# Performance work log

Measured on AMD Instinct MI355X. Metric: run time of the kernel, lower is better.

The kernel has to match this reference:

```python
import jax, jax.numpy as jnp
import numpy as np
from jax import lax

B, P, DMAX, DMEL, H = 32, 192, 48, 80, 64
BN_EPS = 1e-5


def setup_inputs() -> dict:
    key = jax.random.key(0)
    ks = jax.random.split(key, 20)
    T = P * DMAX
    s = 0.1
    k_gru = 1.0 / np.sqrt(H)
    inp = {
        "mels": jax.random.normal(ks[0], (B, T, DMEL), jnp.float32),
        # phone durations in frames, in [1, DMAX]
        "durations": jax.random.randint(ks[1], (B, P), 0, DMAX, dtype=jnp.int32) + 1,
        "max_dur": DMAX,
        "conv_w": 1.0 + s * jax.random.normal(ks[2], (2,), jnp.float32),
        "conv_b": s * jax.random.normal(ks[3], (2,), jnp.float32),
        "bn_gamma": 0.5 + jax.random.uniform(ks[4], (2,), jnp.float32),
        "bn_beta": s * jax.random.normal(ks[5], (2,), jnp.float32),
        "bn_mean": s * jax.random.normal(ks[6], (2,), jnp.float32),
        "bn_var": 0.5 + jax.random.uniform(ks[7], (2,), jnp.float32),
        "W_ih_f": k_gru * jax.random.normal(ks[8], (3 * H, DMEL), jnp.float32),
        "W_hh_f": k_gru * jax.random.normal(ks[9], (3 * H, H), jnp.float32),
        "b_ih_f": k_gru * jax.random.normal(ks[10], (3 * H,), jnp.float32),
        "b_hh_f": k_gru * jax.random.normal(ks[11], (3 * H,), jnp.float32),
        "W_ih_b": k_gru * jax.random.normal(ks[12], (3 * H, DMEL), jnp.float32),
        "W_hh_b": k_gru * jax.random.normal(ks[13], (3 * H, H), jnp.float32),
        "b_ih_b": k_gru * jax.random.normal(ks[14], (3 * H,), jnp.float32),
        "b_hh_b": k_gru * jax.random.normal(ks[15], (3 * H,), jnp.float32),
    }
    return inp


def gru_cell(x, h, Wih, Whh, bih, bhh):
    # PyTorch GRU cell convention (gate order r, z, n)
    gi = x @ Wih.T + bih
    gh = h @ Whh.T + bhh
    ir, iz, inn = jnp.split(gi, 3, axis=-1)
    hr, hz, hn = jnp.split(gh, 3, axis=-1)
    r = jax.nn.sigmoid(ir + hr)
    z = jax.nn.sigmoid(iz + hz)
    n = jnp.tanh(inn + r * hn)
    return (1.0 - z) * n + z * h


def reference(mels, durations, max_dur, conv_w, conv_b, bn_gamma, bn_beta,
              bn_mean, bn_var, W_ih_f, W_hh_f, b_ih_f, b_hh_f,
              W_ih_b, W_hh_b, b_ih_b, b_hh_b):
    Bq, T, D = mels.shape
    Pq = durations.shape[1]
    Hq = W_hh_f.shape[1]

    # --- mel2phone: gather each phone's mel segment into [B, P, DMAX, D] ---
    ends = jnp.cumsum(durations, axis=1)
    starts = ends - durations
    t = jnp.arange(max_dur)
    idx = jnp.clip(starts[:, :, None] + t[None, None, :], 0, T - 1)  # [B,P,Dmax]
    segs = mels[jnp.arange(Bq)[:, None, None], idx]                  # [B,P,Dmax,D]
    mask = t[None, None, :] < durations[:, :, None]                  # [B,P,Dmax]

    # --- ConvBNorms2d: 1x1 single-channel conv + eval-mode BN + ReLU, x n_layers ---
    x = segs
    for i in range(conv_w.shape[0]):
        x = conv_w[i] * x + conv_b[i]
        x = (x - bn_mean[i]) * (bn_gamma[i] / jnp.sqrt(bn_var[i] + BN_EPS)) + bn_beta[i]
        x = jax.nn.relu(x)

    # --- per-segment bidirectional GRU, keep last valid timestep ---
    BP = Bq * Pq
    xs = x.reshape(BP, max_dur, D).transpose(1, 0, 2)        # [Dmax, BP, D]
    ms = mask.reshape(BP, max_dur).T                         # [Dmax, BP]

    def step(h, inp):
        xt, mt = inp
        hn = gru_cell(xt, h, W_ih_f, W_hh_f, b_ih_f, b_hh_f)
        h = jnp.where(mt[:, None], hn, h)  # freeze hidden past segment end
        return h, None

    h0 = jnp.zeros((BP, Hq), x.dtype)
    h_fwd, _ = lax.scan(step, h0, (xs, ms))                  # fwd hidden at len-1

    # backward direction output at the last valid position = one GRU step on x[len-1]
    last_idx = jnp.clip(durations - 1, 0, max_dur - 1)       # [B,P]
    x_last = jnp.take_along_axis(x, last_idx[:, :, None, None], axis=2)[:, :, 0, :]
    h_bwd = gru_cell(x_last.reshape(BP, D), h0, W_ih_b, W_hh_b, b_ih_b, b_hh_b)

    out = jnp.concatenate([h_fwd, h_bwd], axis=-1).reshape(Bq, Pq, 2 * Hq)
    out = out * (durations > 0)[:, :, None]  # phone2utter zero-padding
    return out


if __name__ == "__main__":
    o = reference(**setup_inputs())
    print(o.shape, o.dtype)
```

## Files before the change

kernel.cpp:

```cpp
#include <hip/hip_runtime.h>

#define NB 32
#define NP 192
#define DM 48
#define ND 80
#define NH 64
#define NT (NP*DM)
#define NBP (NB*NP)
#define NSG (NBP/16)

typedef _Float16 half8 __attribute__((ext_vector_type(8)));
typedef float f32x4 __attribute__((ext_vector_type(4)));

#define WS_STARTS 0
#define WS_WIH   32768
#define WS_WHH   (32768 + 36864)
#define WS_WIHB  (32768 + 36864 + 24576)

__device__ __forceinline__ float sigm(float x){ return 1.0f/(1.0f + __expf(-x)); }
__device__ __forceinline__ float tanh_f(float x){ return 1.0f - 2.0f/(1.0f + __expf(2.0f*x)); }

__device__ __forceinline__ unsigned packh2(float a, float b){
    unsigned short ua = __builtin_bit_cast(unsigned short, (_Float16)a);
    unsigned short ub = __builtin_bit_cast(unsigned short, (_Float16)b);
    return (unsigned)ua | ((unsigned)ub << 16);
}

struct Aff { float a0,c0,a1,c1; };
__device__ __forceinline__ Aff make_aff(const float* cw, const float* cb, const float* bg,
                                        const float* bb, const float* bm, const float* bv){
    float s0 = bg[0]*rsqrtf(bv[0]+1e-5f);
    float s1 = bg[1]*rsqrtf(bv[1]+1e-5f);
    Aff A;
    A.a0 = cw[0]*s0; A.c0 = (cb[0]-bm[0])*s0 + bb[0];
    A.a1 = cw[1]*s1; A.c1 = (cb[1]-bm[1])*s1 + bb[1];
    return A;
}
__device__ __forceinline__ float aff(float x, const Aff A){
    float y = fmaxf(fmaf(A.a0, x, A.c0), 0.0f);
    return fmaxf(fmaf(A.a1, y, A.c1), 0.0f);
}

__device__ __forceinline__ void lds_barrier(){
    asm volatile("s_waitcnt lgkmcnt(0)" ::: "memory");
    __builtin_amdgcn_s_barrier();
    asm volatile("" ::: "memory");
}

__global__ __launch_bounds__(NP) void k_starts(const int* __restrict__ dur,
                                               int* __restrict__ starts){
    __shared__ int s[NP];
    int b = blockIdx.x, p = threadIdx.x;
    int d = dur[b*NP + p];
    s[p] = d;
    __syncthreads();
    #pragma unroll
    for (int off = 1; off < NP; off <<= 1){
        int v = (p >= off) ? s[p - off] : 0;
        __syncthreads();
        s[p] += v;
        __syncthreads();
    }
    starts[b*NP + p] = s[p] - d;
}

__global__ __launch_bounds__(256) void k_prep(const float* __restrict__ Wih,
                                              const float* __restrict__ Whh,
                                              const float* __restrict__ Wihb,
                                              unsigned short* __restrict__ wih16,
                                              unsigned short* __restrict__ whh16,
                                              unsigned short* __restrict__ wihb16){
    int idx = blockIdx.x*256 + threadIdx.x;
    if (idx < 12*3*64*8){
        int i = idx & 7, l = (idx>>3) & 63, ks = (idx>>9) % 3, f = idx / 1536;
        int j = (f>>2)*64 + (f&3)*16 + (l&15);
        int k = ks*32 + (l>>4)*8 + i;
        float v = (k < ND) ? Wih[j*ND + k] : 0.0f;
        wih16[idx] = __builtin_bit_cast(unsigned short, (_Float16)v);
        return;
    }
    int idx2 = idx - 12*3*64*8;
    if (idx2 < 12*2*64*8){
        int i = idx2 & 7, l = (idx2>>3) & 63, ks = (idx2>>9) & 1, f = idx2 / 1024;
        int j = (f>>2)*64 + (f&3)*16 + (l&15);
        int k = ks*32 + (l>>4)*8 + i;
        whh16[idx2] = __builtin_bit_cast(unsigned short, (_Float16)Whh[j*NH + k]);
        return;
    }
    int idx3 = idx2 - 12*2*64*8;
    if (idx3 < 12*3*64*8){
        int i = idx3 & 7, l = (idx3>>3) & 63, ks = (idx3>>9) % 3, f = idx3 / 1536;
        int j = (f>>2)*64 + (f&3)*16 + (l&15);
        int k = ks*32 + (l>>4)*8 + i;
        float v = (k < ND) ? Wihb[j*ND + k] : 0.0f;
        wihb16[idx3] = __builtin_bit_cast(unsigned short, (_Float16)v);
    }
}

__global__ __launch_bounds__(256, 2) void k_fused(
        const float* __restrict__ mels,
        const int* __restrict__ starts,
        const int* __restrict__ dur,
        const unsigned short* __restrict__ wih16,
        const unsigned short* __restrict__ whh16,
        const unsigned short* __restrict__ wihb16,
        const float* __restrict__ bih,  const float* __restrict__ bhh,
        const float* __restrict__ bihb, const float* __restrict__ bhhb,
        const float* __restrict__ cw, const float* __restrict__ cb,
        const float* __restrict__ bg, const float* __restrict__ bb,
        const float* __restrict__ bm, const float* __restrict__ bv,
        float* __restrict__ out){
    __shared__ alignas(16) uint4 xf[3*192];
    __shared__ alignas(16) uint4 xlast[192];
    __shared__ alignas(16) unsigned short hh2[2*1152];
    __shared__ alignas(16) unsigned short hl2[2*1152];

    int sg  = blockIdx.x;
    int tid = threadIdx.x;
    int w = tid >> 6, l = tid & 63;
    int sc = l & 15, g4 = l >> 4;
    Aff A = make_aff(cw,cb,bg,bb,bm,bv);

    half8 Af[3][3], Ah[3][2];
    #pragma unroll
    for (int gt = 0; gt < 3; ++gt){
        #pragma unroll
        for (int ks = 0; ks < 3; ++ks)
            Af[gt][ks] = *(const half8*)(wih16 + (size_t)(((gt*4+w)*3 + ks)*64 + l)*8);
        #pragma unroll
        for (int ks = 0; ks < 2; ++ks)
            Ah[gt][ks] = *(const half8*)(whh16 + (size_t)(((gt*4+w)*2 + ks)*64 + l)*8);
    }
    f32x4 bi[3], bh[3];
    #pragma unroll
    for (int gt = 0; gt < 3; ++gt){
        float4 t4 = *(const float4*)(bih + gt*64 + w*16 + g4*4);
        bi[gt][0]=t4.x; bi[gt][1]=t4.y; bi[gt][2]=t4.z; bi[gt][3]=t4.w;
        float4 u4 = *(const float4*)(bhh + gt*64 + w*16 + g4*4);
        bh[gt][0]=u4.x; bh[gt][1]=u4.y; bh[gt][2]=u4.z; bh[gt][3]=u4.w;
    }
    int dl_g = dur[sg*16 + sc];

    bool stg = (tid < 192);
    int ks_s = tid >> 6, ls = tid & 63;
    int scs = ls & 15, g4s = ls >> 4;
    int k0 = ks_s*32 + g4s*8;
    bool valid = stg && (k0 < ND);
    int st_s = 0, d_s = -1;
    if (stg){ st_s = starts[sg*16 + scs]; d_s = dur[sg*16 + scs]; }
    const float* mb = mels + (size_t)(sg/12)*NT*ND;

    auto ld2 = [&](int t, float4& va, float4& vb){
        int r = st_s + t; r = (r < NT-1) ? r : (NT-1);
        const float* p = mb + (size_t)r*ND + k0;
        va = *(const float4*)p;
        vb = *(const float4*)(p + 4);
    };
    auto stage = [&](int pw, int tt, float4 va, float4 vb){
        if (valid){
            float y0=aff(va.x,A), y1=aff(va.y,A), y2=aff(va.z,A), y3=aff(va.w,A);
            float y4=aff(vb.x,A), y5=aff(vb.y,A), y6=aff(vb.z,A), y7=aff(vb.w,A);
            uint4 P = uint4{packh2(y0,y1), packh2(y2,y3), packh2(y4,y5), packh2(y6,y7)};
            xf[pw*192 + tid] = P;
            if (tt == d_s - 1) xlast[tid] = P;
        }
    };

    if (stg && !valid){
        uint4 z = uint4{0,0,0,0};
        xf[0*192 + tid] = z; xf[1*192 + tid] = z; xf[2*192 + tid] = z;
        xlast[tid] = z;
    }
    for (int i = tid; i < 288; i += 256){
        ((uint4*)hh2)[i] = uint4{0,0,0,0};
        ((uint4*)hl2)[i] = uint4{0,0,0,0};
    }
    float4 va0 = {0,0,0,0}, vb0 = {0,0,0,0}, va1 = {0,0,0,0}, vb1 = {0,0,0,0};
    if (valid) ld2(0, va0, vb0);
    stage(0, 0, va0, vb0);
    if (valid) ld2(1, va0, vb0);
    float h[4] = {0.f,0.f,0.f,0.f};
    lds_barrier();

#define MFMA(a,b,c) __builtin_amdgcn_mfma_f32_16x16x32_f16(a,b,c,0,0,0)
#define GSTEP(K, SA, SB, LA, LB)                                                      \
{                                                                                     \
    const int PR = (K) % 3, PW = ((K)+1) % 3, HB = (K) & 1;                           \
    const int t = tb + (K);                                                           \
    half8 X0  = *(const half8*)&xf[PR*192 +   0 + l];                                 \
    half8 X1  = *(const half8*)&xf[PR*192 +  64 + l];                                 \
    half8 X2  = *(const half8*)&xf[PR*192 + 128 + l];                                 \
    half8 Hh0 = *(const half8*)&hh2[HB*1152 + sc*72 +  0 + g4*8];                     \
    half8 Hh1 = *(const half8*)&hh2[HB*1152 + sc*72 + 32 + g4*8];                     \
    half8 Hl0 = *(const half8*)&hl2[HB*1152 + sc*72 +  0 + g4*8];                     \
    half8 Hl1 = *(const half8*)&hl2[HB*1152 + sc*72 + 32 + g4*8];                     \
    if (t+1 < DM) stage(PW, t+1, SA, SB);                                             \
    if (valid && (t+2 < DM)) ld2(t+2, LA, LB);                                        \
    f32x4 ga0 = bi[0], ga1 = bi[1], ga2 = bi[2];                                      \
    f32x4 ha0 = bh[0], ha1 = bh[1], ha2 = bh[2];                                      \
    ha0 = MFMA(Ah[0][0], Hh0, ha0); ha1 = MFMA(Ah[1][0], Hh0, ha1);                   \
    ha2 = MFMA(Ah[2][0], Hh0, ha2);                                                   \
    ga0 = MFMA(Af[0][0], X0, ga0);  ga1 = MFMA(Af[1][0], X0, ga1);                    \
    ga2 = MFMA(Af[2][0], X0, ga2);                                                    \
    ha0 = MFMA(Ah[0][0], Hl0, ha0); ha1 = MFMA(Ah[1][0], Hl0, ha1);                   \
    ha2 = MFMA(Ah[2][0], Hl0, ha2);                                                   \
    ga0 = MFMA(Af[0][1], X1, ga0);  ga1 = MFMA(Af[1][1], X1, ga1);                    \
    ga2 = MFMA(Af[2][1], X1, ga2);                                                    \
    ha0 = MFMA(Ah[0][1], Hh1, ha0); ha1 = MFMA(Ah[1][1], Hh1, ha1);                   \
    ha2 = MFMA(Ah[2][1], Hh1, ha2);                                                   \
    ha0 = MFMA(Ah[0][1], Hl1, ha0); ha1 = MFMA(Ah[1][1], Hl1, ha1);                   \
    ha2 = MFMA(Ah[2][1], Hl1, ha2);                                                   \
    ga0 = MFMA(Af[0][2], X2, ga0);  ga1 = MFMA(Af[1][2], X2, ga1);                    \
    ga2 = MFMA(Af[2][2], X2, ga2);                                                    \
    _Pragma("unroll")                                                                 \
    for (int r = 0; r < 4; ++r){                                                      \
        float rr = sigm(ga0[r] + ha0[r]);                                             \
        float zz = sigm(ga1[r] + ha1[r]);                                             \
        float nn = tanh_f(ga2[r] + rr*ha2[r]);                                        \
        float hn2 = (1.0f - zz)*nn + zz*h[r];                                         \
        h[r] = (t < dl_g) ? hn2 : h[r];                                               \
    }                                                                                 \
    { float e0 = h[0]-(float)(_Float16)h[0], e1 = h[1]-(float)(_Float16)h[1];         \
      float e2 = h[2]-(float)(_Float16)h[2], e3 = h[3]-(float)(_Float16)h[3];         \
      *(uint2*)&hh2[(HB^1)*1152 + sc*72 + w*16 + g4*4] =                              \
          uint2{packh2(h[0],h[1]), packh2(h[2],h[3])};                                \
      *(uint2*)&hl2[(HB^1)*1152 + sc*72 + w*16 + g4*4] =                              \
          uint2{packh2(e0,e1), packh2(e2,e3)};                                        \
    }                                                                                 \
    lds_barrier();                                                                    \
}

    for (int tb = 0; tb < DM; tb += 6){
        GSTEP(0, va0, vb0, va1, vb1)
        GSTEP(1, va1, vb1, va0, vb0)
        GSTEP(2, va0, vb0, va1, vb1)
        GSTEP(3, va1, vb1, va0, vb0)
        GSTEP(4, va0, vb0, va1, vb1)
        GSTEP(5, va1, vb1, va0, vb0)
    }
#undef GSTEP

    float mk = (dl_g > 0) ? 1.0f : 0.0f;
    {
        float4 o4 = {h[0]*mk, h[1]*mk, h[2]*mk, h[3]*mk};
        *(float4*)(out + ((size_t)sg*16 + sc)*(2*NH) + w*16 + g4*4) = o4;
    }

    half8 Afb[3][3];
    #pragma unroll
    for (int gt = 0; gt < 3; ++gt)
        #pragma unroll
        for (int ks = 0; ks < 3; ++ks)
            Afb[gt][ks] = *(const half8*)(wihb16 + (size_t)(((gt*4+w)*3 + ks)*64 + l)*8);
    f32x4 ab0, ab1, ab2;
    {
        float4 t0 = *(const float4*)(bihb + 0*64 + w*16 + g4*4);
        float4 t1 = *(const float4*)(bihb + 1*64 + w*16 + g4*4);
        float4 t2 = *(const float4*)(bihb + 2*64 + w*16 + g4*4);
        ab0[0]=t0.x; ab0[1]=t0.y; ab0[2]=t0.z; ab0[3]=t0.w;
        ab1[0]=t1.x; ab1[1]=t1.y; ab1[2]=t1.z; ab1[3]=t1.w;
        ab2[0]=t2.x; ab2[1]=t2.y; ab2[2]=t2.z; ab2[3]=t2.w;
    }
    #pragma unroll
    for (int ks = 0; ks < 3; ++ks){
        half8 Bx = *(const half8*)&xlast[ks*64 + l];
        ab0 = MFMA(Afb[0][ks], Bx, ab0);
        ab1 = MFMA(Afb[1][ks], Bx, ab1);
        ab2 = MFMA(Afb[2][ks], Bx, ab2);
    }
    {
        float4 p0 = *(const float4*)(bhhb + 0*64 + w*16 + g4*4);
        float4 p1 = *(const float4*)(bhhb + 1*64 + w*16 + g4*4);
        float4 p2 = *(const float4*)(bhhb + 2*64 + w*16 + g4*4);
        float pr0[4] = {p0.x,p0.y,p0.z,p0.w};
        float pr1[4] = {p1.x,p1.y,p1.z,p1.w};
        float pr2[4] = {p2.x,p2.y,p2.z,p2.w};
        float ho[4];
        #pragma unroll
        for (int r = 0; r < 4; ++r){
            float rr = sigm(ab0[r] + pr0[r]);
            float zz = sigm(ab1[r] + pr1[r]);
            float nn = tanh_f(ab2[r] + rr*pr2[r]);
            ho[r] = (1.0f - zz)*nn * mk;
        }
        float4 o4 = {ho[0], ho[1], ho[2], ho[3]};
        *(float4*)(out + ((size_t)sg*16 + sc)*(2*NH) + NH + w*16 + g4*4) = o4;
    }
#undef MFMA
}

extern "C" void kernel_launch(void* const* d_in, const int* in_sizes, int n_in,
                              void* d_out, int out_size, void* d_ws, size_t ws_size,
                              hipStream_t stream){
    const float* mels = (const float*)d_in[0];
    const int*   dur  = (const int*)d_in[1];
    const float* cw = (const float*)d_in[3];
    const float* cb = (const float*)d_in[4];
    const float* bg = (const float*)d_in[5];
    const float* bb = (const float*)d_in[6];
    const float* bm = (const float*)d_in[7];
    const float* bv = (const float*)d_in[8];
    const float* Wihf = (const float*)d_in[9];
    const float* Whhf = (const float*)d_in[10];
    const float* bihf = (const float*)d_in[11];
    const float* bhhf = (const float*)d_in[12];
    const float* Wihb = (const float*)d_in[13];
    const float* bihb = (const float*)d_in[15];
    const float* bhhb = (const float*)d_in[16];
    float* out = (float*)d_out;

    int*            starts = (int*)((char*)d_ws + WS_STARTS);
    unsigned short* wih16  = (unsigned short*)((char*)d_ws + WS_WIH);
    unsigned short* whh16  = (unsigned short*)((char*)d_ws + WS_WHH);
    unsigned short* wihb16 = (unsigned short*)((char*)d_ws + WS_WIHB);

    k_starts<<<NB, NP, 0, stream>>>(dur, starts);
    k_prep<<<192, 256, 0, stream>>>(Wihf, Whhf, Wihb, wih16, whh16, wihb16);
    k_fused<<<NSG, 256, 0, stream>>>(mels, starts, dur, wih16, whh16, wihb16,
                                     bihf, bhhf, bihb, bhhb,
                                     cw, cb, bg, bb, bm, bv, out);
}
```

Before: 220.0 us.

## Precompute fp16 activations in a fused prep kernel and drop hidden-state split precision

Merges the starts-scan and weight-prep kernels into one launch that also applies the conv/BN/ReLU affine to all mels and writes them as padded fp16 rows to workspace. The recurrent kernel then streams 16-byte fp16 rows instead of fp32 pairs and skips the per-step affine math. It also drops the hi/lo split of the hidden state, halving the recurrent MFMAs and LDS traffic per step. In exchange there is an extra full pass over mels plus a workspace write and read, and reduced precision in the h@Whh product, which may hurt accuracy.

New measurement: 233.3 us. 1.06x slower.

```diff
diff --git a/kernel.cpp b/kernel.cpp
--- a/kernel.cpp
+++ b/kernel.cpp
@@ -8,6 +8,7 @@
 #define NT (NP*DM)
 #define NBP (NB*NP)
 #define NSG (NBP/16)
+#define NR (NB*NT)
 
 typedef _Float16 half8 __attribute__((ext_vector_type(8)));
 typedef float f32x4 __attribute__((ext_vector_type(4)));
@@ -16,6 +17,7 @@
 #define WS_WIH   32768
 #define WS_WHH   (32768 + 36864)
 #define WS_WIHB  (32768 + 36864 + 24576)
+#define WS_XG    (256*1024)
 
 __device__ __forceinline__ float sigm(float x){ return 1.0f/(1.0f + __expf(-x)); }
 __device__ __forceinline__ float tanh_f(float x){ return 1.0f - 2.0f/(1.0f + __expf(2.0f*x)); }
@@ -47,58 +49,82 @@
     asm volatile("" ::: "memory");
 }
 
-__global__ __launch_bounds__(NP) void k_starts(const int* __restrict__ dur,
-                                               int* __restrict__ starts){
-    __shared__ int s[NP];
-    int b = blockIdx.x, p = threadIdx.x;
-    int d = dur[b*NP + p];
-    s[p] = d;
-    __syncthreads();
-    #pragma unroll
-    for (int off = 1; off < NP; off <<= 1){
-        int v = (p >= off) ? s[p - off] : 0;
+__global__ __launch_bounds__(256) void k_pre(
+        const int* __restrict__ dur, int* __restrict__ starts,
+        const float* __restrict__ Wih, const float* __restrict__ Whh,
+        const float* __restrict__ Wihb,
+        unsigned short* __restrict__ wih16, unsigned short* __restrict__ whh16,
+        unsigned short* __restrict__ wihb16,
+        const float* __restrict__ mels, unsigned short* __restrict__ xg,
+        const float* __restrict__ cw, const float* __restrict__ cb,
+        const float* __restrict__ bg, const float* __restrict__ bb,
+        const float* __restrict__ bm, const float* __restrict__ bv){
+    int blk = blockIdx.x, tid = threadIdx.x;
+    if (blk < NB){
+        __shared__ int s[NP];
+        int d = 0;
+        if (tid < NP){ d = dur[blk*NP + tid]; s[tid] = d; }
         __syncthreads();
-        s[p] += v;
-        __syncthreads();
-    }
-    starts[b*NP + p] = s[p] - d;
-}
-
-__global__ __launch_bounds__(256) void k_prep(const float* __restrict__ Wih,
-                                              const float* __restrict__ Whh,
-                                              const float* __restrict__ Wihb,
-                                              unsigned short* __restrict__ wih16,
-                                              unsigned short* __restrict__ whh16,
-                                              unsigned short* __restrict__ wihb16){
-    int idx = blockIdx.x*256 + threadIdx.x;
-    if (idx < 12*3*64*8){
-        int i = idx & 7, l = (idx>>3) & 63, ks = (idx>>9) % 3, f = idx / 1536;
-        int j = (f>>2)*64 + (f&3)*16 + (l&15);
-        int k = ks*32 + (l>>4)*8 + i;
-        float v = (k < ND) ? Wih[j*ND + k] : 0.0f;
-        wih16[idx] = __builtin_bit_cast(unsigned short, (_Float16)v);
+        #pragma unroll
+        for (int off = 1; off < NP; off <<= 1){
+            int v = (tid >= off && tid < NP) ? s[tid - off] : 0;
+            __syncthreads();
+            if (tid < NP) s[tid] += v;
+            __syncthreads();
+        }
+        if (tid < NP) starts[blk*NP + tid] = s[tid] - d;
         return;
     }
-    int idx2 = idx - 12*3*64*8;
-    if (idx2 < 12*2*64*8){
-        int i = idx2 & 7, l = (idx2>>3) & 63, ks = (idx2>>9) & 1, f = idx2 / 1024;
-        int j = (f>>2)*64 + (f&3)*16 + (l&15);
-        int k = ks*32 + (l>>4)*8 + i;
-        whh16[idx2] = __builtin_bit_cast(unsigned short, (_Float16)Whh[j*NH + k]);
+    if (blk < NB + 192){
+        int idx = (blk - NB)*256 + tid;
+        if (idx < 12*3*64*8){
+            int i = idx & 7, l = (idx>>3) & 63, ks = (idx>>9) % 3, f = idx / 1536;
+            int j = (f>>2)*64 + (f&3)*16 + (l&15);
+            int k = ks*32 + (l>>4)*8 + i;
+            float v = (k < ND) ? Wih[j*ND + k] : 0.0f;
+            wih16[idx] = __builtin_bit_cast(unsigned short, (_Float16)v);
+            return;
+        }
+        int idx2 = idx - 12*3*64*8;
+        if (idx2 < 12*2*64*8){
+            int i = idx2 & 7, l = (idx2>>3) & 63, ks = (idx2>>9) & 1, f = idx2 / 1024;
+            int j = (f>>2)*64 + (f&3)*16 + (l&15);
+            int k = ks*32 + (l>>4)*8 + i;
+            whh16[idx2] = __builtin_bit_cast(unsigned short, (_Float16)Whh[j*NH + k]);
+            return;
+        }
+        int idx3 = idx2 - 12*2*64*8;
+        if (idx3 < 12*3*64*8){
+            int i = idx3 & 7, l = (idx3>>3) & 63, ks = (idx3>>9) % 3, f = idx3 / 1536;
+            int j = (f>>2)*64 + (f&3)*16 + (l&15);
+            int k = ks*32 + (l>>4)*8 + i;
+            float v = (k < ND) ? Wihb[j*ND + k] : 0.0f;
+            wihb16[idx3] = __builtin_bit_cast(unsigned short, (_Float16)v);
+        }
         return;
     }
-    int idx3 = idx2 - 12*2*64*8;
-    if (idx3 < 12*3*64*8){
-        int i = idx3 & 7, l = (idx3>>3) & 63, ks = (idx3>>9) % 3, f = idx3 / 1536;
-        int j = (f>>2)*64 + (f&3)*16 + (l&15);
-        int k = ks*32 + (l>>4)*8 + i;
-        float v = (k < ND) ? Wihb[j*ND + k] : 0.0f;
-        wihb16[idx3] = __builtin_bit_cast(unsigned short, (_Float16)v);
+    Aff A = make_aff(cw,cb,bg,bb,bm,bv);
+    int u0 = (blk - (NB+192))*256 + tid;
+    int stride = (gridDim.x - (NB+192))*256;
+    for (int u = u0; u < NR*12; u += stride){
+        int R = u / 12, kb = u % 12, k0 = kb*8;
+        uint4 P;
+        if (k0 < ND){
+            const float* p = mels + (size_t)R*ND + k0;
+            float4 a = *(const float4*)p;
+            float4 b4 = *(const float4*)(p + 4);
+            float y0=aff(a.x,A),  y1=aff(a.y,A),  y2=aff(a.z,A),  y3=aff(a.w,A);
+            float y4=aff(b4.x,A), y5=aff(b4.y,A), y6=aff(b4.z,A), y7=aff(b4.w,A);
+            P = uint4{packh2(y0,y1), packh2(y2,y3), packh2(y4,y5), packh2(y6,y7)};
+        } else {
+            P = uint4{0u,0u,0u,0u};
+        }
+        *(uint4*)(xg + (size_t)R*96 + k0) = P;
     }
 }
 
 __global__ __launch_bounds__(256, 2) void k_fused(
-        const float* __restrict__ mels,
+        const unsigned short* __restrict__ xg,
         const int* __restrict__ starts,
         const int* __restrict__ dur,
         const unsigned short* __restrict__ wih16,
@@ -106,20 +132,15 @@
         const unsigned short* __restrict__ wihb16,
         const float* __restrict__ bih,  const float* __restrict__ bhh,
         const float* __restrict__ bihb, const float* __restrict__ bhhb,
-        const float* __restrict__ cw, const float* __restrict__ cb,
-        const float* __restrict__ bg, const float* __restrict__ bb,
-        const float* __restrict__ bm, const float* __restrict__ bv,
         float* __restrict__ out){
     __shared__ alignas(16) uint4 xf[3*192];
     __shared__ alignas(16) uint4 xlast[192];
     __shared__ alignas(16) unsigned short hh2[2*1152];
-    __shared__ alignas(16) unsigned short hl2[2*1152];
 
     int sg  = blockIdx.x;
     int tid = threadIdx.x;
     int w = tid >> 6, l = tid & 63;
     int sc = l & 15, g4 = l >> 4;
-    Aff A = make_aff(cw,cb,bg,bb,bm,bv);
 
     half8 Af[3][3], Ah[3][2];
     #pragma unroll
@@ -145,45 +166,29 @@
     int ks_s = tid >> 6, ls = tid & 63;
     int scs = ls & 15, g4s = ls >> 4;
     int k0 = ks_s*32 + g4s*8;
-    bool valid = stg && (k0 < ND);
     int st_s = 0, d_s = -1;
     if (stg){ st_s = starts[sg*16 + scs]; d_s = dur[sg*16 + scs]; }
-    const float* mb = mels + (size_t)(sg/12)*NT*ND;
-
-    auto ld2 = [&](int t, float4& va, float4& vb){
+    const unsigned short* xgb = xg + (size_t)(sg/12)*NT*96;
+
+    auto ldx = [&](int t) -> uint4 {
         int r = st_s + t; r = (r < NT-1) ? r : (NT-1);
-        const float* p = mb + (size_t)r*ND + k0;
-        va = *(const float4*)p;
-        vb = *(const float4*)(p + 4);
+        return *(const uint4*)(xgb + (size_t)r*96 + k0);
     };
-    auto stage = [&](int pw, int tt, float4 va, float4 vb){
-        if (valid){
-            float y0=aff(va.x,A), y1=aff(va.y,A), y2=aff(va.z,A), y3=aff(va.w,A);
-            float y4=aff(vb.x,A), y5=aff(vb.y,A), y6=aff(vb.z,A), y7=aff(vb.w,A);
-            uint4 P = uint4{packh2(y0,y1), packh2(y2,y3), packh2(y4,y5), packh2(y6,y7)};
-            xf[pw*192 + tid] = P;
-            if (tt == d_s - 1) xlast[tid] = P;
-        }
-    };
-
-    if (stg && !valid){
-        uint4 z = uint4{0,0,0,0};
-        xf[0*192 + tid] = z; xf[1*192 + tid] = z; xf[2*192 + tid] = z;
-        xlast[tid] = z;
-    }
-    for (int i = tid; i < 288; i += 256){
-        ((uint4*)hh2)[i] = uint4{0,0,0,0};
-        ((uint4*)hl2)[i] = uint4{0,0,0,0};
-    }
-    float4 va0 = {0,0,0,0}, vb0 = {0,0,0,0}, va1 = {0,0,0,0}, vb1 = {0,0,0,0};
-    if (valid) ld2(0, va0, vb0);
-    stage(0, 0, va0, vb0);
-    if (valid) ld2(1, va0, vb0);
+
+    for (int i = tid; i < 144; i += 256)
+        ((uint4*)hh2)[i] = uint4{0u,0u,0u,0u};
+    uint4 Pa = {0u,0u,0u,0u}, Pb = {0u,0u,0u,0u};
+    if (stg){
+        Pa = ldx(0);
+        xf[tid] = Pa;
+        if (0 == d_s - 1) xlast[tid] = Pa;
+        Pa = ldx(1);
+    }
     float h[4] = {0.f,0.f,0.f,0.f};
     lds_barrier();
 
 #define MFMA(a,b,c) __builtin_amdgcn_mfma_f32_16x16x32_f16(a,b,c,0,0,0)
-#define GSTEP(K, SA, SB, LA, LB)                                                      \
+#define GSTEP(K, PC, PN)                                                              \
 {                                                                                     \
     const int PR = (K) % 3, PW = ((K)+1) % 3, HB = (K) & 1;                           \
     const int t = tb + (K);                                                           \
@@ -192,24 +197,21 @@
     half8 X2  = *(const half8*)&xf[PR*192 + 128 + l];                                 \
     half8 Hh0 = *(const half8*)&hh2[HB*1152 + sc*72 +  0 + g4*8];                     \
     half8 Hh1 = *(const half8*)&hh2[HB*1152 + sc*72 + 32 + g4*8];                     \
-    half8 Hl0 = *(const half8*)&hl2[HB*1152 + sc*72 +  0 + g4*8];                     \
-    half8 Hl1 = *(const half8*)&hl2[HB*1152 + sc*72 + 32 + g4*8];                     \
-    if (t+1 < DM) stage(PW, t+1, SA, SB);                                             \
-    if (valid && (t+2 < DM)) ld2(t+2, LA, LB);                                        \
+    if (stg && (t+1 < DM)){                                                           \
+        xf[PW*192 + tid] = PC;                                                        \
+        if ((t+1) == d_s - 1) xlast[tid] = PC;                                        \
+    }                                                                                 \
+    if (stg && (t+2 < DM)) PN = ldx(t+2);                                             \
     f32x4 ga0 = bi[0], ga1 = bi[1], ga2 = bi[2];                                      \
     f32x4 ha0 = bh[0], ha1 = bh[1], ha2 = bh[2];                                      \
     ha0 = MFMA(Ah[0][0], Hh0, ha0); ha1 = MFMA(Ah[1][0], Hh0, ha1);                   \
     ha2 = MFMA(Ah[2][0], Hh0, ha2);                                                   \
     ga0 = MFMA(Af[0][0], X0, ga0);  ga1 = MFMA(Af[1][0], X0, ga1);                    \
     ga2 = MFMA(Af[2][0], X0, ga2);                                                    \
-    ha0 = MFMA(Ah[0][0], Hl0, ha0); ha1 = MFMA(Ah[1][0], Hl0, ha1);                   \
-    ha2 = MFMA(Ah[2][0], Hl0, ha2);                                                   \
+    ha0 = MFMA(Ah[0][1], Hh1, ha0); ha1 = MFMA(Ah[1][1], Hh1, ha1);                   \
+    ha2 = MFMA(Ah[2][1], Hh1, ha2);                                                   \
     ga0 = MFMA(Af[0][1], X1, ga0);  ga1 = MFMA(Af[1][1], X1, ga1);                    \
     ga2 = MFMA(Af[2][1], X1, ga2);                                                    \
-    ha0 = MFMA(Ah[0][1], Hh1, ha0); ha1 = MFMA(Ah[1][1], Hh1, ha1);                   \
-    ha2 = MFMA(Ah[2][1], Hh1, ha2);                                                   \
-    ha0 = MFMA(Ah[0][1], Hl1, ha0); ha1 = MFMA(Ah[1][1], Hl1, ha1);                   \
-    ha2 = MFMA(Ah[2][1], Hl1, ha2);                                                   \
     ga0 = MFMA(Af[0][2], X2, ga0);  ga1 = MFMA(Af[1][2], X2, ga1);                    \
     ga2 = MFMA(Af[2][2], X2, ga2);                                                    \
     _Pragma("unroll")                                                                 \
@@ -220,23 +222,18 @@
         float hn2 = (1.0f - zz)*nn + zz*h[r];                                         \
         h[r] = (t < dl_g) ? hn2 : h[r];                                               \
     }                                                                                 \
-    { float e0 = h[0]-(float)(_Float16)h[0], e1 = h[1]-(float)(_Float16)h[1];         \
-      float e2 = h[2]-(float)(_Float16)h[2], e3 = h[3]-(float)(_Float16)h[3];         \
-      *(uint2*)&hh2[(HB^1)*1152 + sc*72 + w*16 + g4*4] =                              \
-          uint2{packh2(h[0],h[1]), packh2(h[2],h[3])};                                \
-      *(uint2*)&hl2[(HB^1)*1152 + sc*72 + w*16 + g4*4] =                              \
-          uint2{packh2(e0,e1), packh2(e2,e3)};                                        \
-    }                                                                                 \
+    *(uint2*)&hh2[(HB^1)*1152 + sc*72 + w*16 + g4*4] =                                \
+        uint2{packh2(h[0],h[1]), packh2(h[2],h[3])};                                  \
     lds_barrier();                                                                    \
 }
 
     for (int tb = 0; tb < DM; tb += 6){
-        GSTEP(0, va0, vb0, va1, vb1)
-        GSTEP(1, va1, vb1, va0, vb0)
-        GSTEP(2, va0, vb0, va1, vb1)
-        GSTEP(3, va1, vb1, va0, vb0)
-        GSTEP(4, va0, vb0, va1, vb1)
-        GSTEP(5, va1, vb1, va0, vb0)
+        GSTEP(0, Pa, Pb)
+        GSTEP(1, Pb, Pa)
+        GSTEP(2, Pa, Pb)
+        GSTEP(3, Pb, Pa)
+        GSTEP(4, Pa, Pb)
+        GSTEP(5, Pb, Pa)
     }
 #undef GSTEP
 
@@ -313,10 +310,11 @@
     unsigned short* wih16  = (unsigned short*)((char*)d_ws + WS_WIH);
     unsigned short* whh16  = (unsigned short*)((char*)d_ws + WS_WHH);
     unsigned short* wihb16 = (unsigned short*)((char*)d_ws + WS_WIHB);
-
-    k_starts<<<NB, NP, 0, stream>>>(dur, starts);
-    k_prep<<<192, 256, 0, stream>>>(Wihf, Whhf, Wihb, wih16, whh16, wihb16);
-    k_fused<<<NSG, 256, 0, stream>>>(mels, starts, dur, wih16, whh16, wihb16,
-                                     bihf, bhhf, bihb, bhhb,
-                                     cw, cb, bg, bb, bm, bv, out);
-}
+    unsigned short* xg     = (unsigned short*)((char*)d_ws + WS_XG);
+
+    k_pre<<<NB + 192 + 1024, 256, 0, stream>>>(dur, starts, Wihf, Whhf, Wihb,
+                                               wih16, whh16, wihb16, mels, xg,
+                                               cw, cb, bg, bb, bm, bv);
+    k_fused<<<NSG, 256, 0, stream>>>(xg, starts, dur, wih16, whh16, wihb16,
+                                     bihf, bhhf, bihb, bhhb, out);
+}
```
